# Optimization experiments

Hardware: AMD Instinct MI355X
Metric: run time of the kernel (lower is better)

The kernel has to match this reference:

```python
import jax, jax.numpy as jnp
import numpy as np

COMMITMENT_COST = 0.25
ENTROPY_LOSS_WEIGHT = 0.1
EPSILON = 1e-05
NUM_EMBEDDINGS = 2048
EMBEDDING_DIM = 64


def setup_inputs() -> dict:
    key = jax.random.key(0)
    kx, ke = jax.random.split(key)
    x = jax.random.normal(kx, (16, 64, 64, EMBEDDING_DIM), dtype=jnp.float32)
    embedding = jax.random.normal(ke, (NUM_EMBEDDINGS, EMBEDDING_DIM), dtype=jnp.float32)
    return {"x": x, "embedding": embedding}


def reference(x, embedding):
    input_shape = x.shape
    flat_x = x.reshape(-1, EMBEDDING_DIM)              # [N, D]
    distances = (jnp.sum(flat_x ** 2, axis=1, keepdims=True)
                 + jnp.sum(embedding ** 2, axis=1)
                 - 2.0 * jnp.matmul(flat_x, embedding.T))
    encoding_indices = jnp.argmin(distances, axis=1)   # [N]
    quantized = embedding[encoding_indices].reshape(input_shape)

    commitment_loss = jnp.mean((jax.lax.stop_gradient(quantized) - x) ** 2)
    codebook_loss = jnp.mean((quantized - jax.lax.stop_gradient(x)) ** 2)
    # straight-through estimator
    quantized = x + jax.lax.stop_gradient(quantized - x)

    # histogram of code usage == mean of one-hot encodings (scatter-add, avoids [N,K] one-hot)
    n_tokens = flat_x.shape[0]
    counts = jnp.zeros((NUM_EMBEDDINGS,), dtype=flat_x.dtype).at[encoding_indices].add(1.0)
    avg_probs = counts / n_tokens
    perplexity = jnp.exp(-jnp.sum(avg_probs * jnp.log(avg_probs + EPSILON)))
    entropy_loss = jnp.sum(avg_probs * jnp.log(avg_probs + EPSILON))

    vq_loss = codebook_loss + COMMITMENT_COST * commitment_loss + ENTROPY_LOSS_WEIGHT * entropy_loss
    return (quantized, vq_loss, commitment_loss, codebook_loss, perplexity,
            entropy_loss, encoding_indices.reshape(input_shape[:-1]), avg_probs)
```

## Files before the change

kernel.cpp:

```cpp
#include <hip/hip_runtime.h>
#include <float.h>

typedef _Float16 half8 __attribute__((ext_vector_type(8)));
typedef float    f32x4 __attribute__((ext_vector_type(4)));

constexpr int N_TOK = 65536;
constexpr int D     = 64;
constexpr int K     = 2048;
constexpr int TILE_C = 64;
constexpr int NTILE  = K / TILE_C;
constexpr int TOK_PER_BLK = 64;
constexpr int NBLK = N_TOK / TOK_PER_BLK;
constexpr float EPS_RESCORE = 0.15f;

constexpr size_t QN       = (size_t)N_TOK * D;
constexpr size_t SCAL_OFF = QN;
constexpr size_t IDX_OFF  = QN + 5;
constexpr size_t PROB_OFF = IDX_OFF + N_TOK;

constexpr size_t WS_HNORM = 0;
constexpr size_t WS_COUNT = 8192;
constexpr size_t WS_BSUM  = 16384;
constexpr size_t WS_SW    = 24576;
constexpr int REC_B  = 40;
constexpr int TILE_B = 256 * REC_B;

__device__ inline unsigned long long pack_key(float d, int k) {
    unsigned u = __float_as_uint(d);
    u = (u & 0x80000000u) ? ~u : (u | 0x80000000u);
    return ((unsigned long long)u << 32) | (unsigned)k;
}

__device__ inline float unpack_dist(unsigned long long key) {
    unsigned u = (unsigned)(key >> 32);
    u = (u & 0x80000000u) ? (u & 0x7FFFFFFFu) : ~u;
    return __uint_as_float(u);
}

__device__ inline unsigned long long shfl_xor_u64_w16(unsigned long long v, int m) {
    int lo = __shfl_xor((int)(unsigned)v, m, 16);
    int hi = __shfl_xor((int)(unsigned)(v >> 32), m, 16);
    return ((unsigned long long)(unsigned)hi << 32) | (unsigned)lo;
}

__global__ __launch_bounds__(256) void vq_init(const float* __restrict__ emb,
                                               float* __restrict__ hnorm,
                                               unsigned* __restrict__ counts,
                                               double* __restrict__ blocksums,
                                               char* __restrict__ swb) {
    const int g  = blockIdx.x * 256 + threadIdx.x;
    const int r  = g >> 3;
    const int c0 = g & 7;
    const float4* p4 = (const float4*)(emb + (size_t)r * D + 8 * c0);
    float4 q0 = p4[0], q1 = p4[1];
    float v[8] = {q0.x, q0.y, q0.z, q0.w, q1.x, q1.y, q1.z, q1.w};
    half8 h;
    float s = 0.f;
#pragma unroll
    for (int i = 0; i < 8; ++i) {
        s += v[i] * v[i];
        h[i] = (_Float16)v[i];
    }
    const int t    = r >> 6;
    const int w    = (r >> 4) & 3;
    const int m16  = r & 15;
    const int lane = (c0 & 3) * 16 + m16;
    const int slot = c0 >> 2;
    char* rec = swb + (size_t)(t * 256 + w * 64 + lane) * REC_B;
    *(half8*)(rec + slot * 16) = h;

#pragma unroll
    for (int off = 1; off < 8; off <<= 1) s += __shfl_xor(s, off, 8);
    if (c0 < 4) *(float*)(rec + 32) = 0.5f * s;
    if (c0 == 0) hnorm[r] = 0.5f * s;
    if (g < K) counts[g] = 0u;
    if (g < NBLK) blocksums[g] = 0.0;
}

#define ISSUE(P0, P1, HN, SB)                                                      \
  asm volatile("global_load_dwordx4 %0, %3, %4\n\t"                                \
               "global_load_dwordx4 %1, %3, %4 offset:16\n\t"                      \
               "global_load_dword   %2, %3, %4 offset:32"                          \
               : "=&v"(P0), "=&v"(P1), "=&v"(HN)                                   \
               : "v"(voff), "s"(SB));

#define WAITC(N)                                                                   \
  asm volatile("s_waitcnt vmcnt(" #N ")" ::: "memory");                            \
  __builtin_amdgcn_sched_barrier(0);

#define VQ_STEP(P0, P1, HN, TT)                                                    \
  {                                                                                \
    f32x4 acc[4];                                                                  \
    _Pragma("unroll")                                                              \
    for (int a = 0; a < 4; ++a) {                                                  \
      acc[a] = (f32x4){(HN), (HN), (HN), (HN)};                                    \
      acc[a] = __builtin_amdgcn_mfma_f32_16x16x32_f16(axh[a][0], P0, acc[a], 0, 0, 0); \
      acc[a] = __builtin_amdgcn_mfma_f32_16x16x32_f16(axh[a][1], P1, acc[a], 0, 0, 0); \
    }                                                                              \
    _Pragma("unroll")                                                              \
    for (int a = 0; a < 4; ++a)                                                    \
      _Pragma("unroll")                                                            \
      for (int r = 0; r < 4; ++r) {                                                \
        unsigned _kb = (__float_as_uint(acc[a][r]) & 0xFFFFFFE0u) | (unsigned)(TT);\
        float _f = __uint_as_float(_kb);                                           \
        best2[a][r] = __builtin_amdgcn_fmed3f(best1[a][r], best2[a][r], _f);       \
        best1[a][r] = fminf(best1[a][r], _f);                                      \
      }                                                                            \
  }

__global__ __launch_bounds__(256, 2) void vq_fused(const float* __restrict__ x,
                                                   const float* __restrict__ emb,
                                                   const float* __restrict__ hnorm,
                                                   const char* __restrict__ swb,
                                                   unsigned* __restrict__ counts,
                                                   double* __restrict__ blocksums,
                                                   float* __restrict__ out) {
    __shared__ unsigned long long kls[64][10];
    __shared__ int bks[64];
    __shared__ double wsum[4];

    const int tid  = threadIdx.x;
    const int lane = tid & 63;
    const int wav  = tid >> 6;
    const int t0   = blockIdx.x * TOK_PER_BLK;
    const int m16  = lane & 15;
    const int g    = lane >> 4;
    const int ko   = g * 8;
    const int cit  = wav * 16 + m16;

    half8 axh[4][2];
#pragma unroll
    for (int a = 0; a < 4; ++a) {
        const float* xr = x + (size_t)(t0 + 16 * a + m16) * D;
#pragma unroll
        for (int c = 0; c < 2; ++c) {
            const float4* p4 = (const float4*)(xr + 32 * c + ko);
            float4 q0 = p4[0], q1 = p4[1];
            float v[8] = {q0.x, q0.y, q0.z, q0.w, q1.x, q1.y, q1.z, q1.w};
            half8 h;
#pragma unroll
            for (int j = 0; j < 8; ++j) h[j] = (_Float16)(-v[j]);
            axh[a][c] = h;
        }
    }

    float best1[4][4], best2[4][4];
#pragma unroll
    for (int a = 0; a < 4; ++a)
#pragma unroll
        for (int r = 0; r < 4; ++r) { best1[a][r] = FLT_MAX; best2[a][r] = FLT_MAX; }

    const unsigned voff = (unsigned)(tid * REC_B);
    unsigned long long sb = (unsigned long long)swb;

    half8 A0, A1;  float hA;
    half8 B0, B1;  float hB;
    half8 C0, C1;  float hC;
    half8 D0, D1;  float hD;

    ISSUE(A0, A1, hA, sb); sb += TILE_B;
    ISSUE(B0, B1, hB, sb); sb += TILE_B;
    ISSUE(C0, C1, hC, sb); sb += TILE_B;

    for (int t = 0; t < 28; t += 4) {
        ISSUE(D0, D1, hD, sb); sb += TILE_B;
        WAITC(9);
        VQ_STEP(A0, A1, hA, t);
        ISSUE(A0, A1, hA, sb); sb += TILE_B;
        WAITC(9);
        VQ_STEP(B0, B1, hB, t + 1);
        ISSUE(B0, B1, hB, sb); sb += TILE_B;
        WAITC(9);
        VQ_STEP(C0, C1, hC, t + 2);
        ISSUE(C0, C1, hC, sb); sb += TILE_B;
        WAITC(9);
        VQ_STEP(D0, D1, hD, t + 3);
    }
    ISSUE(D0, D1, hD, sb);
    WAITC(9);
    VQ_STEP(A0, A1, hA, 28);
    WAITC(6);
    VQ_STEP(B0, B1, hB, 29);
    WAITC(3);
    VQ_STEP(C0, C1, hC, 30);
    WAITC(0);
    VQ_STEP(D0, D1, hD, 31);

#pragma unroll
    for (int a = 0; a < 4; ++a)
#pragma unroll
        for (int r = 0; r < 4; ++r) {
            const unsigned b1 = __float_as_uint(best1[a][r]);
            const unsigned b2 = __float_as_uint(best2[a][r]);
            unsigned long long k1 = pack_key(best1[a][r], (int)(b1 & 31u) * TILE_C + cit);
            unsigned long long k2 = pack_key(best2[a][r], (int)(b2 & 31u) * TILE_C + cit);
#pragma unroll
            for (int off = 8; off; off >>= 1) {
                unsigned long long o1 = shfl_xor_u64_w16(k1, off);
                unsigned long long o2 = shfl_xor_u64_w16(k2, off);
                unsigned long long hi1 = (k1 > o1) ? k1 : o1;
                unsigned long long lo2 = (k2 < o2) ? k2 : o2;
                k1 = (k1 < o1) ? k1 : o1;
                k2 = (hi1 < lo2) ? hi1 : lo2;
            }
            if (m16 == 0) {
                kls[16 * a + g * 4 + r][wav]     = k1;
                kls[16 * a + g * 4 + r][4 + wav] = k2;
            }
        }
    __syncthreads();

    if (tid < 64) {
        float ds[8]; int kk[8];
        unsigned long long kmin = ~0ULL;
#pragma unroll
        for (int w = 0; w < 8; ++w) {
            unsigned long long key = kls[tid][w];
            ds[w] = unpack_dist(key);
            kk[w] = (int)(unsigned)(key & 0xFFFFFFFFu);
            if (key < kmin) kmin = key;
        }
        int bk = (int)(unsigned)(kmin & 0xFFFFFFFFu);
        const float fmin = unpack_dist(kmin);
        int cnt = 0;
#pragma unroll
        for (int w = 0; w < 8; ++w) cnt += (ds[w] <= fmin + EPS_RESCORE) ? 1 : 0;

        if (cnt > 1) {
            unsigned long long bkey = ~0ULL;
            const float* xr = x + (size_t)(t0 + tid) * D;
            for (int w = 0; w < 8; ++w) {
                if (ds[w] <= fmin + EPS_RESCORE) {
                    const int k = kk[w];
                    const float* cr = emb + (size_t)k * D;
                    float s0 = 0.f, s1 = 0.f, s2 = 0.f, s3 = 0.f;
#pragma unroll
                    for (int i = 0; i < 16; ++i) {
                        s0 = fmaf(cr[4 * i + 0], xr[4 * i + 0], s0);
                        s1 = fmaf(cr[4 * i + 1], xr[4 * i + 1], s1);
                        s2 = fmaf(cr[4 * i + 2], xr[4 * i + 2], s2);
                        s3 = fmaf(cr[4 * i + 3], xr[4 * i + 3], s3);
                    }
                    float hd = hnorm[k] - ((s0 + s1) + (s2 + s3));
                    unsigned long long key = pack_key(hd, k);
                    if (key < bkey) bkey = key;
                }
            }
            bk = (int)(unsigned)(bkey & 0xFFFFFFFFu);
        }
        bks[tid] = bk;
        out[IDX_OFF + t0 + tid] = (float)bk;
        atomicAdd(&counts[bk], 1u);
    }
    __syncthreads();

    const int tok = tid >> 2;
    const int i4  = tid & 3;
    const int bk  = bks[tok];
    const float4* xr4 = (const float4*)(x + (size_t)(t0 + tok) * D);
    const float4* cr4 = (const float4*)(emb + (size_t)bk * D);
    float4* qr4 = (float4*)(out + (size_t)(t0 + tok) * D);
    float local = 0.f;
#pragma unroll
    for (int ii = 0; ii < 4; ++ii) {
        const int idx = i4 + 4 * ii;
        float4 xv = xr4[idx];
        float4 cv = cr4[idx];
        float dx = cv.x - xv.x, dy = cv.y - xv.y;
        float dz = cv.z - xv.z, dw = cv.w - xv.w;
        local += dx * dx + dy * dy + dz * dz + dw * dw;
        float4 q;
        q.x = xv.x + dx; q.y = xv.y + dy;
        q.z = xv.z + dz; q.w = xv.w + dw;
        qr4[idx] = q;
    }
    double ld = (double)local;
#pragma unroll
    for (int off = 32; off > 0; off >>= 1) ld += __shfl_down(ld, off, 64);
    if (lane == 0) wsum[wav] = ld;
    __syncthreads();
    if (tid == 0)
        blocksums[blockIdx.x] = (wsum[0] + wsum[1]) + (wsum[2] + wsum[3]);
}

__global__ __launch_bounds__(256) void vq_finalize(const unsigned* __restrict__ counts,
                                                   const double* __restrict__ blocksums,
                                                   float* __restrict__ out) {
    const int tid = threadIdx.x;
    double e = 0.0;
#pragma unroll
    for (int i = 0; i < 8; ++i) {
        int k = tid + i * 256;
        float p = (float)counts[k] / 65536.0f;
        out[PROB_OFF + k] = p;
        double pd = (double)p;
        e += pd * log(pd + 1e-5);
    }
    double s = 0.0;
#pragma unroll
    for (int i = 0; i < NBLK / 256; ++i) s += blocksums[tid + i * 256];
#pragma unroll
    for (int off = 32; off > 0; off >>= 1) {
        e += __shfl_down(e, off, 64);
        s += __shfl_down(s, off, 64);
    }
    __shared__ double we[4], ws2[4];
    int lane = tid & 63, wid = tid >> 6;
    if (lane == 0) { we[wid] = e; ws2[wid] = s; }
    __syncthreads();
    if (tid == 0) {
        double entropy = (we[0] + we[1]) + (we[2] + we[3]);
        double sumsq   = (ws2[0] + ws2[1]) + (ws2[2] + ws2[3]);
        double mse     = sumsq / (double)((size_t)N_TOK * D);
        out[SCAL_OFF + 0] = (float)(1.25 * mse + 0.1 * entropy);
        out[SCAL_OFF + 1] = (float)mse;
        out[SCAL_OFF + 2] = (float)mse;
        out[SCAL_OFF + 3] = (float)exp(-entropy);
        out[SCAL_OFF + 4] = (float)entropy;
    }
}

extern "C" void kernel_launch(void* const* d_in, const int* in_sizes, int n_in,
                              void* d_out, int out_size, void* d_ws, size_t ws_size,
                              hipStream_t stream) {
    const float* x   = (const float*)d_in[0];
    const float* emb = (const float*)d_in[1];
    float* out = (float*)d_out;

    char* ws = (char*)d_ws;
    float*    hnorm     = (float*)(ws + WS_HNORM);
    unsigned* counts    = (unsigned*)(ws + WS_COUNT);
    double*   blocksums = (double*)(ws + WS_BSUM);
    char*     swb       = ws + WS_SW;

    vq_init<<<K * 8 / 256, 256, 0, stream>>>(emb, hnorm, counts, blocksums, swb);
    vq_fused<<<NBLK, 256, 0, stream>>>(x, emb, hnorm, swb, counts, blocksums, out);
    vq_finalize<<<1, 256, 0, stream>>>(counts, blocksums, out);
}
```

Before: 129.0 us.

## Software-pipeline MFMA and argmin compare across alternating accumulator sets

Splits each tile step into an MFMA phase and a compare phase. Two accumulator sets (even and odd) let tile t+1's MFMAs be issued before tile t's top-2 min update. The aim is to hide MFMA latency behind the VALU compare work rather than stalling on each accumulator's result. This costs 16 more accumulator VGPRs under a 2-waves-per-SIMD launch bound, which could cause spills or scheduling issues.

```diff
diff --git a/kernel.cpp b/kernel.cpp
--- a/kernel.cpp
+++ b/kernel.cpp
@@ -88,25 +88,26 @@
   asm volatile("s_waitcnt vmcnt(" #N ")" ::: "memory");                            \
   __builtin_amdgcn_sched_barrier(0);
 
-#define VQ_STEP(P0, P1, HN, TT)                                                    \
+#define VQ_MFMA(P0, P1, HN, ACC)                                                   \
   {                                                                                \
-    f32x4 acc[4];                                                                  \
+    f32x4 _hv = {(HN), (HN), (HN), (HN)};                                          \
     _Pragma("unroll")                                                              \
     for (int a = 0; a < 4; ++a) {                                                  \
-      acc[a] = (f32x4){(HN), (HN), (HN), (HN)};                                    \
-      acc[a] = __builtin_amdgcn_mfma_f32_16x16x32_f16(axh[a][0], P0, acc[a], 0, 0, 0); \
-      acc[a] = __builtin_amdgcn_mfma_f32_16x16x32_f16(axh[a][1], P1, acc[a], 0, 0, 0); \
+      ACC[a] = __builtin_amdgcn_mfma_f32_16x16x32_f16(axh[a][0], P0, _hv, 0, 0, 0);    \
+      ACC[a] = __builtin_amdgcn_mfma_f32_16x16x32_f16(axh[a][1], P1, ACC[a], 0, 0, 0); \
     }                                                                              \
+  }
+
+#define VQ_CMP(ACC, TT)                                                            \
     _Pragma("unroll")                                                              \
     for (int a = 0; a < 4; ++a)                                                    \
       _Pragma("unroll")                                                            \
       for (int r = 0; r < 4; ++r) {                                                \
-        unsigned _kb = (__float_as_uint(acc[a][r]) & 0xFFFFFFE0u) | (unsigned)(TT);\
+        unsigned _kb = (__float_as_uint(ACC[a][r]) & 0xFFFFFFE0u) | (unsigned)(TT);\
         float _f = __uint_as_float(_kb);                                           \
         best2[a][r] = __builtin_amdgcn_fmed3f(best1[a][r], best2[a][r], _f);       \
         best1[a][r] = fminf(best1[a][r], _f);                                      \
-      }                                                                            \
-  }
+      }
 
 __global__ __launch_bounds__(256, 2) void vq_fused(const float* __restrict__ x,
                                                    const float* __restrict__ emb,
@@ -157,34 +158,44 @@
     half8 B0, B1;  float hB;
     half8 C0, C1;  float hC;
     half8 D0, D1;  float hD;
+    f32x4 accE[4], accO[4];
 
     ISSUE(A0, A1, hA, sb); sb += TILE_B;
     ISSUE(B0, B1, hB, sb); sb += TILE_B;
     ISSUE(C0, C1, hC, sb); sb += TILE_B;
 
-    for (int t = 0; t < 28; t += 4) {
+    ISSUE(D0, D1, hD, sb); sb += TILE_B;
+    WAITC(9);
+    VQ_MFMA(A0, A1, hA, accE);
+
+    for (int t = 1; t < 26; t += 4) {
+        ISSUE(A0, A1, hA, sb); sb += TILE_B;
+        WAITC(9);
+        VQ_MFMA(B0, B1, hB, accO);
+        VQ_CMP(accE, t - 1);
+        ISSUE(B0, B1, hB, sb); sb += TILE_B;
+        WAITC(9);
+        VQ_MFMA(C0, C1, hC, accE);
+        VQ_CMP(accO, t);
+        ISSUE(C0, C1, hC, sb); sb += TILE_B;
+        WAITC(9);
+        VQ_MFMA(D0, D1, hD, accO);
+        VQ_CMP(accE, t + 1);
         ISSUE(D0, D1, hD, sb); sb += TILE_B;
         WAITC(9);
-        VQ_STEP(A0, A1, hA, t);
-        ISSUE(A0, A1, hA, sb); sb += TILE_B;
-        WAITC(9);
-        VQ_STEP(B0, B1, hB, t + 1);
-        ISSUE(B0, B1, hB, sb); sb += TILE_B;
-        WAITC(9);
-        VQ_STEP(C0, C1, hC, t + 2);
-        ISSUE(C0, C1, hC, sb); sb += TILE_B;
-        WAITC(9);
-        VQ_STEP(D0, D1, hD, t + 3);
-    }
-    ISSUE(D0, D1, hD, sb);
-    WAITC(9);
-    VQ_STEP(A0, A1, hA, 28);
+        VQ_MFMA(A0, A1, hA, accE);
+        VQ_CMP(accO, t + 2);
+    }
     WAITC(6);
-    VQ_STEP(B0, B1, hB, 29);
+    VQ_MFMA(B0, B1, hB, accO);
+    VQ_CMP(accE, 28);
     WAITC(3);
-    VQ_STEP(C0, C1, hC, 30);
+    VQ_MFMA(C0, C1, hC, accE);
+    VQ_CMP(accO, 29);
     WAITC(0);
-    VQ_STEP(D0, D1, hD, 31);
+    VQ_MFMA(D0, D1, hD, accO);
+    VQ_CMP(accE, 30);
+    VQ_CMP(accO, 31);
 
 #pragma unroll
     for (int a = 0; a < 4; ++a)
```

Measured after the change: 123.2 us. -4.5%, faster.
